# Kernel tuning notes

Measured on AMD Instinct MI355X. Metric: run time of the kernel, lower is better.

## Reference

```python
import jax, jax.numpy as jnp
import numpy as np

# Izhikevich parameters (regular spiking defaults)
A = 0.02     # recovery time scale
B = 0.2      # sensitivity of recovery
C = -65.0    # reset voltage
D = 8.0      # recovery reset increment
VTH = 30.0   # spike threshold
BETA = 1.0   # surrogate gradient sharpness
DT = 0.5     # integration time step (ms)


@jax.custom_vjp
def spike_fn(v):
    # Heaviside forward, surrogate sigmoid-derivative backward
    return (v >= VTH).astype(v.dtype)

def _spike_fwd(v):
    return spike_fn(v), v

def _spike_bwd(v, g):
    s = jax.nn.sigmoid(BETA * (v - VTH))
    return (g * (BETA * s * (1.0 - s)),)

spike_fn.defvjp(_spike_fwd, _spike_bwd)


def setup_inputs() -> dict:
    key = jax.random.key(0)
    input_current = jax.random.normal(key, (32, 2000, 512), dtype=jnp.float32)
    return {"input_current": input_current}


def reference(input_current):
    # input_current: [batch, n_steps, n_neurons]
    batch, n_steps, n_neurons = input_current.shape
    dtype = input_current.dtype
    v0 = jnp.full((batch, n_neurons), C, dtype=dtype)
    u0 = jnp.full((batch, n_neurons), B * C, dtype=dtype)

    def step(carry, i_t):
        v, u = carry
        dv = (0.04 * v * v + 5.0 * v + 140.0 - u + i_t) * DT
        du = A * (B * v - u) * DT
        v = v + dv
        u = u + du
        s = spike_fn(v)
        v = v * (1.0 - s) + C * s
        u = u + D * s
        return (v, u), (s, v, u)

    xs = jnp.swapaxes(input_current, 0, 1)  # [n_steps, batch, n_neurons]
    _, (spikes, voltages, recovery) = jax.lax.scan(step, (v0, u0), xs)
    # back to [batch, n_steps, n_neurons]
    spikes = jnp.swapaxes(spikes, 0, 1)
    voltages = jnp.swapaxes(voltages, 0, 1)
    recovery = jnp.swapaxes(recovery, 0, 1)
    return spikes, voltages, recovery
```

## Files before the change

### kernel.cpp

```cpp
#include <hip/hip_runtime.h>


#define NSTEPS 2000
#define NNEUR  512
#define BATCH  32
#define INPLANE 1024000u
#define PLANE  32768000u
#define CHUNK  100
#define NCHUNK (NSTEPS / CHUNK)
#define NG     (CHUNK / 4)

typedef const __attribute__((address_space(1))) unsigned GPtr;
typedef __attribute__((address_space(3))) unsigned LPtr;

__device__ __forceinline__ void izh_step(float i_t, float& v, float& u, float& s) {
#pragma clang fp contract(off)
    float t1 = 0.04f * v;
    t1 = t1 * v;
    float t2 = 5.0f * v;
    float acc = t1 + t2;
    acc = acc + 140.0f;
    acc = acc - u;
    acc = acc + i_t;
    float dv = acc * 0.5f;
    float t4 = 0.2f * v;
    t4 = t4 - u;
    t4 = 0.02f * t4;
    float du = t4 * 0.5f;
    v = v + dv;
    u = u + du;
    bool sp = (v >= 30.0f);
    s = sp ? 1.0f : 0.0f;
    v = sp ? -65.0f : v;
    u = sp ? (u + 8.0f) : u;
}

__global__ __launch_bounds__(64, 1) void izh_kernel(const float* __restrict__ in,
                                                    float* __restrict__ out) {
    __shared__ float lds[2][CHUNK * 64];

    const int lane = threadIdx.x;
    const int gid  = blockIdx.x * 64 + lane;
    const unsigned b  = (unsigned)(gid >> 9);
    const unsigned n  = (unsigned)(gid & (NNEUR - 1));
    const unsigned n0 = (unsigned)((blockIdx.x * 64) & (NNEUR - 1));

    const float* gsrc = in + (size_t)b * INPLANE
                           + (size_t)(lane >> 4) * NNEUR
                           + n0 + (size_t)(lane & 15) * 4;

    unsigned voff = b * INPLANE + n;

    float v = -65.0f;
    float u = -13.0f;

#pragma unroll
    for (int g = 0; g < NG; ++g) {
        __builtin_amdgcn_global_load_lds((GPtr*)(gsrc + (size_t)(4 * g) * NNEUR),
                                         (LPtr*)&lds[0][g * 256], 16, 0, 0);
    }

    for (int c = 0; c < NCHUNK; ++c) {
        asm volatile("s_waitcnt vmcnt(0)" ::: "memory");

        if (c + 1 < NCHUNK) {
            const float* gs = gsrc + (size_t)(c + 1) * CHUNK * NNEUR;
            float* lb = &lds[(c + 1) & 1][0];
#pragma unroll
            for (int g = 0; g < NG; ++g) {
                __builtin_amdgcn_global_load_lds((GPtr*)(gs + (size_t)(4 * g) * NNEUR),
                                                 (LPtr*)(lb + g * 256), 16, 0, 0);
            }
        }

        const float* lbuf = &lds[c & 1][0];
        float ra[4], rb[4];
#pragma unroll
        for (int j = 0; j < 4; ++j) ra[j] = lbuf[j * 64 + lane];

        for (int g = 0; g < NG - 1; g += 2) {
#pragma unroll
            for (int j = 0; j < 4; ++j) rb[j] = lbuf[(4 * (g + 1) + j) * 64 + lane];
#pragma unroll
            for (int j = 0; j < 4; ++j) {
                float s;
                izh_step(ra[j], v, u, s);
                out[voff] = s;
                out[voff + PLANE] = v;
                out[voff + 2u * PLANE] = u;
                voff += NNEUR;
            }
            if (g + 2 < NG) {
#pragma unroll
                for (int j = 0; j < 4; ++j) ra[j] = lbuf[(4 * (g + 2) + j) * 64 + lane];
            }
#pragma unroll
            for (int j = 0; j < 4; ++j) {
                float s;
                izh_step(rb[j], v, u, s);
                out[voff] = s;
                out[voff + PLANE] = v;
                out[voff + 2u * PLANE] = u;
                voff += NNEUR;
            }
        }
#pragma unroll
        for (int j = 0; j < 4; ++j) {
            float s;
            izh_step(ra[j], v, u, s);
            out[voff] = s;
            out[voff + PLANE] = v;
            out[voff + 2u * PLANE] = u;
            voff += NNEUR;
        }
    }
}

extern "C" void kernel_launch(void* const* d_in, const int* in_sizes, int n_in,
                              void* d_out, int out_size, void* d_ws, size_t ws_size,
                              hipStream_t stream) {
    const float* in = (const float*)d_in[0];
    float* out = (float*)d_out;
    izh_kernel<<<(BATCH * NNEUR) / 64, 64, 0, stream>>>(in, out);
}
```

Before: 526.3 us.

## Split Izhikevich kernel into producer wave and three per-output compute waves

The block grows from one wave to four. One wave streams input chunks into double-buffered LDS, and three waves each redundantly run the neuron recurrence but store only one of the spike, voltage or recovery planes. Work-group barriers per chunk coordinate the buffers. This spreads the store traffic across more waves per CU to hide memory latency, at the cost of triplicated arithmetic and per-chunk barrier synchronization.

```diff
diff --git a/kernel.cpp b/kernel.cpp
--- a/kernel.cpp
+++ b/kernel.cpp
@@ -35,45 +35,16 @@
     u = sp ? (u + 8.0f) : u;
 }
 
-__global__ __launch_bounds__(64, 1) void izh_kernel(const float* __restrict__ in,
-                                                    float* __restrict__ out) {
-    __shared__ float lds[2][CHUNK * 64];
-
-    const int lane = threadIdx.x;
-    const int gid  = blockIdx.x * 64 + lane;
-    const unsigned b  = (unsigned)(gid >> 9);
-    const unsigned n  = (unsigned)(gid & (NNEUR - 1));
-    const unsigned n0 = (unsigned)((blockIdx.x * 64) & (NNEUR - 1));
-
-    const float* gsrc = in + (size_t)b * INPLANE
-                           + (size_t)(lane >> 4) * NNEUR
-                           + n0 + (size_t)(lane & 15) * 4;
-
-    unsigned voff = b * INPLANE + n;
-
+template <int W>
+__device__ __forceinline__ void run_compute(const float (*lin)[CHUNK * 64], int lane,
+                                            unsigned voff, float* __restrict__ out) {
+    float* oplane = out + (size_t)W * PLANE;
     float v = -65.0f;
     float u = -13.0f;
 
-#pragma unroll
-    for (int g = 0; g < NG; ++g) {
-        __builtin_amdgcn_global_load_lds((GPtr*)(gsrc + (size_t)(4 * g) * NNEUR),
-                                         (LPtr*)&lds[0][g * 256], 16, 0, 0);
-    }
-
+    asm volatile("s_barrier" ::: "memory");
     for (int c = 0; c < NCHUNK; ++c) {
-        asm volatile("s_waitcnt vmcnt(0)" ::: "memory");
-
-        if (c + 1 < NCHUNK) {
-            const float* gs = gsrc + (size_t)(c + 1) * CHUNK * NNEUR;
-            float* lb = &lds[(c + 1) & 1][0];
-#pragma unroll
-            for (int g = 0; g < NG; ++g) {
-                __builtin_amdgcn_global_load_lds((GPtr*)(gs + (size_t)(4 * g) * NNEUR),
-                                                 (LPtr*)(lb + g * 256), 16, 0, 0);
-            }
-        }
-
-        const float* lbuf = &lds[c & 1][0];
+        const float* lbuf = &lin[c & 1][0];
         float ra[4], rb[4];
 #pragma unroll
         for (int j = 0; j < 4; ++j) ra[j] = lbuf[j * 64 + lane];
@@ -85,9 +56,7 @@
             for (int j = 0; j < 4; ++j) {
                 float s;
                 izh_step(ra[j], v, u, s);
-                out[voff] = s;
-                out[voff + PLANE] = v;
-                out[voff + 2u * PLANE] = u;
+                oplane[voff] = (W == 0) ? s : (W == 1) ? v : u;
                 voff += NNEUR;
             }
             if (g + 2 < NG) {
@@ -98,9 +67,7 @@
             for (int j = 0; j < 4; ++j) {
                 float s;
                 izh_step(rb[j], v, u, s);
-                out[voff] = s;
-                out[voff + PLANE] = v;
-                out[voff + 2u * PLANE] = u;
+                oplane[voff] = (W == 0) ? s : (W == 1) ? v : u;
                 voff += NNEUR;
             }
         }
@@ -108,11 +75,53 @@
         for (int j = 0; j < 4; ++j) {
             float s;
             izh_step(ra[j], v, u, s);
-            out[voff] = s;
-            out[voff + PLANE] = v;
-            out[voff + 2u * PLANE] = u;
+            oplane[voff] = (W == 0) ? s : (W == 1) ? v : u;
             voff += NNEUR;
         }
+        asm volatile("s_barrier" ::: "memory");
+    }
+}
+
+__global__ __launch_bounds__(256, 1) void izh_kernel(const float* __restrict__ in,
+                                                     float* __restrict__ out) {
+    __shared__ float lin[2][CHUNK * 64];
+
+    const int tid  = threadIdx.x;
+    const int w    = tid >> 6;
+    const int lane = tid & 63;
+    const unsigned n0 = (unsigned)((blockIdx.x * 64) & (NNEUR - 1));
+    const unsigned b  = (unsigned)((unsigned)(blockIdx.x * 64) >> 9);
+
+    if (w == 3) {
+        const float* gsrc = in + (size_t)b * INPLANE
+                               + (size_t)(lane >> 4) * NNEUR
+                               + n0 + (size_t)(lane & 15) * 4;
+#pragma unroll
+        for (int g = 0; g < NG; ++g) {
+            __builtin_amdgcn_global_load_lds((GPtr*)(gsrc + (size_t)(4 * g) * NNEUR),
+                                             (LPtr*)&lin[0][g * 256], 16, 0, 0);
+        }
+        asm volatile("s_waitcnt vmcnt(0)" ::: "memory");
+        asm volatile("s_barrier" ::: "memory");
+
+        for (int c = 0; c < NCHUNK; ++c) {
+            if (c + 1 < NCHUNK) {
+                const float* gs = gsrc + (size_t)(c + 1) * CHUNK * NNEUR;
+                float* lb = &lin[(c + 1) & 1][0];
+#pragma unroll
+                for (int g = 0; g < NG; ++g) {
+                    __builtin_amdgcn_global_load_lds((GPtr*)(gs + (size_t)(4 * g) * NNEUR),
+                                                     (LPtr*)(lb + g * 256), 16, 0, 0);
+                }
+                asm volatile("s_waitcnt vmcnt(0)" ::: "memory");
+            }
+            asm volatile("s_barrier" ::: "memory");
+        }
+    } else {
+        const unsigned voff0 = b * INPLANE + n0 + (unsigned)lane;
+        if (w == 0)      run_compute<0>(lin, lane, voff0, out);
+        else if (w == 1) run_compute<1>(lin, lane, voff0, out);
+        else             run_compute<2>(lin, lane, voff0, out);
     }
 }
 
@@ -121,5 +130,5 @@
                               hipStream_t stream) {
     const float* in = (const float*)d_in[0];
     float* out = (float*)d_out;
-    izh_kernel<<<(BATCH * NNEUR) / 64, 64, 0, stream>>>(in, out);
+    izh_kernel<<<(BATCH * NNEUR) / 64, 256, 0, stream>>>(in, out);
 }
```

After: 493.0 us. -6.3%, faster.
